# Performance work log

Measured on AMD Instinct MI355X. Metric: run time of the kernel, lower is better.

Reference implementation:

```python
import jax, jax.numpy as jnp
import numpy as np
from jax import lax

B, C, H, W = 32, 3, 128, 128   # batch, image channels, event spatial dims
PC = 16                         # conditioning distribution_params channels
HID = 64                        # hidden channels of each parallel CNN
NUP = 2                         # number of upsampling stages
DN = ('NCHW', 'OIHW', 'NCHW')

BASE_SLICE = (slice(0, None, 2), slice(0, None, 2))
UP_SLICES = [(slice(1, None, 2), slice(1, None, 2)),
             (slice(0, None, 2), slice(1, None, 2)),
             (slice(1, None, 2), slice(0, None, 2))]


def setup_inputs() -> dict:
    key = jax.random.key(0)
    k0, k1, k2, k3 = jax.random.split(key, 4)
    n_nets = C + NUP * 3 * C  # 3 base + 18 upsampling nets = 21
    cin = C + PC
    return {
        'value': jax.random.uniform(k0, (B, C, H, W), jnp.float32),
        'distribution_params': jax.random.normal(k1, (B, PC, H, W), jnp.float32),
        'W1': jax.random.normal(k2, (n_nets, HID, cin, 3, 3), jnp.float32) * 0.05,
        'b1': jnp.zeros((n_nets, HID), jnp.float32),
        'W2': jax.random.normal(k3, (n_nets, 1, HID, 1, 1), jnp.float32) * 0.05,
        'b2': jnp.zeros((n_nets, 1), jnp.float32),
    }


def _cnn(x, w1, bb1, w2, bb2):
    # Conv3x3 -> ReLU -> Conv1x1, producing Bernoulli logits [B,1,h,w]
    h = lax.conv_general_dilated(x, w1, (1, 1), 'SAME', dimension_numbers=DN)
    h = jax.nn.relu(h + bb1[None, :, None, None])
    o = lax.conv_general_dilated(h, w2, (1, 1), 'SAME', dimension_numbers=DN)
    return o + bb2[None, :, None, None]


def _log_prob_block(imgs, params, masked, sl, idxs, W1, b1, W2, b2):
    lp = jnp.float32(0.0)
    for c, idx in enumerate(idxs):
        net_in = jnp.concatenate([masked, params], axis=1)
        logits = _cnn(net_in, W1[idx], b1[idx], W2[idx], b2[idx])[:, 0, sl[0], sl[1]]
        x = imgs[:, c, sl[0], sl[1]]
        # Bernoulli log-prob with logits, summed over batch and spatial dims
        lp = lp + jnp.sum(x * jax.nn.log_sigmoid(logits)
                          + (1.0 - x) * jax.nn.log_sigmoid(-logits))
        masked = masked.at[:, c, sl[0], sl[1]].set(x)
    return lp, masked


def reference(value, distribution_params, W1, b1, W2, b2):
    r = 2 ** NUP
    base = value[:, :, ::r, ::r]
    base_dp = distribution_params[:, :, ::r, ::r]
    masked = jnp.zeros_like(base)
    lp, masked = _log_prob_block(base, base_dp, masked, BASE_SLICE,
                                 list(range(C)), W1, b1, W2, b2)
    for level in range(NUP):
        rr = 2 ** (NUP - level - 1)
        v = value[:, :, ::rr, ::rr]
        dp = distribution_params[:, :, ::rr, ::rr]
        m = jnp.zeros_like(v)
        m = m.at[:, :, BASE_SLICE[0], BASE_SLICE[1]].set(
            v[:, :, BASE_SLICE[0], BASE_SLICE[1]])
        for s in range(3):
            idxs = [C + level * 3 * C + s * C + c for c in range(C)]
            blp, m = _log_prob_block(v, dp, m, UP_SLICES[s], idxs, W1, b1, W2, b2)
            lp = lp + blp
    return lp
```

## Files before the change

### kernel.cpp

```cpp
#include <hip/hip_runtime.h>

typedef unsigned char uchar;
typedef unsigned long long ull;
typedef __attribute__((ext_vector_type(2))) unsigned long long ullx2;
typedef __attribute__((ext_vector_type(4))) float floatx4;
typedef __attribute__((ext_vector_type(4))) unsigned int uintx4;

#define NB_IMG 18496
#define WHALF 9216
#define AREG 16352

__device__ __forceinline__ uchar f2e4(float x) {
    float a = fabsf(x);
    unsigned s = (__float_as_uint(x) >> 24) & 0x80u;
    if (a >= 448.f) return (uchar)(s | 0x7E);
    if (a < 0.015625f) {
        int m = (int)rintf(a * 512.f);
        return (uchar)(s | (unsigned)m);
    }
    unsigned u = __float_as_uint(a);
    unsigned r = u + 0x7FFFFu + ((u >> 20) & 1u);
    unsigned e8 = (r >> 23) - 120u;
    return (uchar)(s | (e8 << 3) | ((r >> 20) & 7u));
}

__device__ __forceinline__ float row16sum(float v) {
    v += __int_as_float(__builtin_amdgcn_update_dpp(0, __float_as_int(v), 0x128, 0xf, 0xf, false));
    v += __int_as_float(__builtin_amdgcn_update_dpp(0, __float_as_int(v), 0x124, 0xf, 0xf, false));
    v += __int_as_float(__builtin_amdgcn_update_dpp(0, __float_as_int(v), 0x122, 0xf, 0xf, false));
    v += __int_as_float(__builtin_amdgcn_update_dpp(0, __float_as_int(v), 0x121, 0xf, 0xf, false));
    return v;
}

__device__ __forceinline__ void eval_geom(int e, int& sy0, int& sx0, int& cch, int& s_idx) {
    if (e < 3) { sy0 = 0; sx0 = 0; cch = e; s_idx = -1; }
    else {
        int u = e - 3; int s = (u % 9) / 3; cch = u % 3; s_idx = s;
        sy0 = (s == 1) ? 0 : 1;
        sx0 = (s == 2) ? 0 : 1;
    }
}

__device__ __forceinline__ bool tap_active(int e, int ci, int dy, int dx,
                                           int sy0, int sx0, int cch, int s_idx) {
    if (ci >= 3) return true;
    int py = (sy0 + dy - 1) & 1;
    int px = (sx0 + dx - 1) & 1;
    if (e < 3) return (py == 0 && px == 0) && (ci < cch);
    if (py == 0 && px == 0) return true;
    int sp = (py == 1 && px == 1) ? 0 : ((py == 0 && px == 1) ? 1 : 2);
    return (sp < s_idx) || (sp == s_idx && ci < cch);
}

__global__ __launch_bounds__(256) void prep_kernel(
    const float* __restrict__ value, const float* __restrict__ dp,
    const float* __restrict__ W1,
    uchar* __restrict__ imgbf, uchar* __restrict__ wbfA, uchar* __restrict__ wbfB,
    float* __restrict__ out)
{
    const int bid = blockIdx.x;
    if (bid < 2312) {
        const int t = bid * 256 + threadIdx.x;
        const int b = t / NB_IMG;
        const int r = t - b * NB_IMG;
        const int y = r / 136;
        const int rr = r - y * 136;
        const int p = rr / 68;
        const int xh = rr - p * 68;
        const int yi = y - 4;
        const int xi = 2 * (xh - 2) + p;
        unsigned d[8];
        #pragma unroll
        for (int i = 0; i < 8; ++i) d[i] = 0;
        if ((unsigned)yi < 128u && (unsigned)xi < 128u) {
            const int o = yi * 128 + xi;
            const float* vb = value + (size_t)b * 3 * 16384 + o;
            const float* pb = dp + (size_t)b * 16 * 16384 + o;
            #pragma unroll
            for (int i = 0; i < 3; ++i) d[i >> 2] |= (unsigned)f2e4(vb[i * 16384]) << ((i & 3) * 8);
            #pragma unroll
            for (int i = 0; i < 16; ++i) {
                const int ci = 3 + i;
                d[ci >> 2] |= (unsigned)f2e4(pb[i * 16384]) << ((ci & 3) * 8);
            }
        }
        uchar* dst = imgbf + (size_t)t * 32;
        uintx4 v0, v1;
        v0[0] = d[0]; v0[1] = d[1]; v0[2] = d[2]; v0[3] = d[3];
        v1[0] = d[4]; v1[1] = d[5]; v1[2] = d[6]; v1[3] = d[7];
        *(uintx4*)dst = v0;
        *(uintx4*)(dst + 16) = v1;
    } else {
        const int q = bid - 2312;
        const int e = q / 9, tap = q % 9;
        const int g = threadIdx.x >> 6, n = threadIdx.x & 63;
        int sy0, sx0, cch, s_idx;
        eval_geom(e, sy0, sx0, cch, s_idx);
        const int dy = tap / 3, dx = tap % 3;
        const float* wrow = W1 + ((size_t)e * 64 + n) * 171;
        ull v = 0;
        #pragma unroll
        for (int qq = 0; qq < 8; ++qq) {
            const int ci = g * 8 + qq;
            float w = 0.f;
            if (ci < 19 && tap_active(e, ci, dy, dx, sy0, sx0, cch, s_idx))
                w = wrow[ci * 9 + tap];
            v |= (ull)f2e4(w) << (qq * 8);
        }
        if (n < 32) *(ull*)&wbfA[(size_t)e * WHALF + ((tap * 4 + g) * 32 + n) * 8] = v;
        else        *(ull*)&wbfB[(size_t)e * WHALF + ((tap * 4 + g) * 32 + (n - 32)) * 8] = v;
        if (bid == 2500 && threadIdx.x == 0) out[0] = 0.f;
    }
}

struct SW { ullx2 a, b, c; };

__device__ __forceinline__ void sw_load(int tid, SW& r, const uchar* wbfB, int e) {
    const uchar* src = wbfB + (size_t)e * WHALF;
    r.a = *(const ullx2*)(src + tid * 16);
    r.b = *(const ullx2*)(src + (256 + tid) * 16);
    if (tid < 64) r.c = *(const ullx2*)(src + (512 + tid) * 16);
}
__device__ __forceinline__ void sw_write(int tid, uchar* dst, const SW& r) {
    *(ullx2*)(dst + tid * 16) = r.a;
    *(ullx2*)(dst + (256 + tid) * 16) = r.b;
    if (tid < 64) *(ullx2*)(dst + (512 + tid) * 16) = r.c;
}

template<int SY0, int SX0, int RSH, int OWSH, int TXH>
__device__ __forceinline__ void class_body(
    int e0, int e_after, SW& sw, float& lpsum,
    int b, int oy0, int ox0, int tid,
    const uchar* Alds, uchar* Wb,
    const uchar* __restrict__ wbfA, const uchar* __restrict__ wbfB,
    const float* __restrict__ value, const float* __restrict__ b1,
    const float* __restrict__ W2, const float* __restrict__ b2)
{
    constexpr int OW = 1 << OWSH;
    const int w = tid >> 6, lane = tid & 63, l15 = lane & 15, l4 = lane >> 4;
    int abase[2];
    #pragma unroll
    for (int a = 0; a < 2; ++a) {
        const int row = w * 32 + a * 16 + l15;
        const int oy = row >> OWSH, ox = row & (OW - 1);
        abase[a] = ((SY0 + 2 * oy) * 2 * TXH + ox) * 24 + l4 * 8;
    }
    const int wfb = l4 * 256 + l15 * 8;

    #pragma unroll 1
    for (int c = 0; c < 3; ++c) {
        const int e = e0 + c;
        const int en = (c < 2) ? (e + 1) : e_after;

        __syncthreads();
        sw_write(tid, Wb, sw);
        if (en >= 0) sw_load(tid, sw, wbfB, en);
        __syncthreads();

        const uchar* wA = wbfA + (size_t)e * WHALF;
        ull breg[9][2];
        #pragma unroll
        for (int tap = 0; tap < 9; ++tap) {
            breg[tap][0] = *(const ull*)(wA + tap * 1024 + wfb);
            breg[tap][1] = *(const ull*)(wA + tap * 1024 + wfb + 128);
        }
        float b1c[4], w2c[4];
        #pragma unroll
        for (int nb = 0; nb < 4; ++nb) {
            b1c[nb] = b1[e * 64 + nb * 16 + l15];
            w2c[nb] = W2[e * 64 + nb * 16 + l15];
        }
        const float bias2 = b2[e];

        floatx4 acc[2][4];
        #pragma unroll
        for (int a = 0; a < 2; ++a)
            #pragma unroll
            for (int nb = 0; nb < 4; ++nb)
                acc[a][nb] = (floatx4){0.f, 0.f, 0.f, 0.f};

        __builtin_amdgcn_s_setprio(1);
        #pragma unroll
        for (int tap = 0; tap < 9; ++tap) {
            const int dy = tap / 3, dx = tap % 3;
            const int v = SX0 + dx + 1;
            const int D = (2 * dy + (v & 1)) * TXH + (v >> 1);
            ull av[2];
            #pragma unroll
            for (int a = 0; a < 2; ++a)
                av[a] = *(const ull*)(Alds + abase[a] + D * 24);
            const ull bv2 = *(const ull*)(Wb + wfb + tap * 1024);
            const ull bv3 = *(const ull*)(Wb + wfb + tap * 1024 + 128);
            #pragma unroll
            for (int a = 0; a < 2; ++a) {
                acc[a][0] = __builtin_amdgcn_mfma_f32_16x16x32_fp8_fp8((long)av[a], (long)breg[tap][0], acc[a][0], 0, 0, 0);
                acc[a][1] = __builtin_amdgcn_mfma_f32_16x16x32_fp8_fp8((long)av[a], (long)breg[tap][1], acc[a][1], 0, 0, 0);
                acc[a][2] = __builtin_amdgcn_mfma_f32_16x16x32_fp8_fp8((long)av[a], (long)bv2, acc[a][2], 0, 0, 0);
                acc[a][3] = __builtin_amdgcn_mfma_f32_16x16x32_fp8_fp8((long)av[a], (long)bv3, acc[a][3], 0, 0, 0);
            }
        }
        __builtin_amdgcn_s_setprio(0);

        float zv[8];
        #pragma unroll
        for (int a = 0; a < 2; ++a)
            #pragma unroll
            for (int j = 0; j < 4; ++j) {
                float part = 0.f;
                #pragma unroll
                for (int nb = 0; nb < 4; ++nb)
                    part += w2c[nb] * fmaxf(acc[a][nb][j] + b1c[nb], 0.f);
                zv[a * 4 + j] = row16sum(part);
            }
        if (l15 < 8) {
            const float u0 = (l15 & 1) ? zv[1] : zv[0];
            const float u1 = (l15 & 1) ? zv[3] : zv[2];
            const float u2 = (l15 & 1) ? zv[5] : zv[4];
            const float u3 = (l15 & 1) ? zv[7] : zv[6];
            const float p0 = (l15 & 2) ? u1 : u0;
            const float p1 = (l15 & 2) ? u3 : u2;
            const float zs = ((l15 & 4) ? p1 : p0) + bias2;
            const int row = w * 32 + ((l15 >> 2) << 4) + (l4 << 2) + (l15 & 3);
            const int oyj = oy0 + (row >> OWSH);
            const int oxj = ox0 + (row & (OW - 1));
            const int yj = (SY0 + 2 * oyj) << RSH;
            const int xj = (SX0 + 2 * oxj) << RSH;
            const float xv = value[((size_t)b * 3 + c) * 16384 + yj * 128 + xj];
            const float az = fabsf(zs);
            const float t2 = __builtin_amdgcn_exp2f(-1.442695041f * az);
            const float l1p = 0.69314718056f * __builtin_amdgcn_logf(1.f + t2);
            lpsum += xv * zs + fminf(-zs, 0.f) - l1p;
        }
    }
}

template<int EB, int RSH, int OWSH, int TXH, int TY, int NCLS>
__device__ __forceinline__ void run_level(
    int b, int oy0, int ox0, int tid,
    uchar* Alds, uchar* Wb, float* wsum,
    const uchar* __restrict__ imgbf, const uchar* __restrict__ wbfA,
    const uchar* __restrict__ wbfB, const float* __restrict__ value,
    const float* __restrict__ b1, const float* __restrict__ W2,
    const float* __restrict__ b2, float* __restrict__ out)
{
    constexpr int TPIX = TY * 2 * TXH;
    const int lane = tid & 63, w = tid >> 6;

    SW sw;
    sw_load(tid, sw, wbfB, EB);

    const int yb = 2 * oy0 - 1, xb = 2 * ox0 - 2;
    const uchar* img_b = imgbf + (size_t)b * ((size_t)NB_IMG * 32);
    #pragma unroll
    for (int i = 0; i < (TPIX + 255) / 256; ++i) {
        const int px = tid + i * 256;
        if (px < TPIX) {
            const int typ = px / TXH;
            const int xh = px - typ * TXH;
            const int yl = yb + (typ >> 1);
            const int xl = xb + 2 * xh + (typ & 1);
            int yi = (yl << RSH) + 4; yi = yi < 0 ? 0 : (yi > 135 ? 135 : yi);
            int xi = (xl << RSH) + 4; xi = xi < 0 ? 0 : (xi > 135 ? 135 : xi);
            const uchar* src = img_b + (size_t)(yi * 136 + (xi & 1) * 68 + (xi >> 1)) * 32;
            ullx2 v01 = *(const ullx2*)src;
            ull v2 = *(const ull*)(src + 16);
            uchar* dst = Alds + px * 24;
            *(ull*)dst = v01[0];
            *(ull*)(dst + 8) = v01[1];
            *(ull*)(dst + 16) = v2;
        }
    }
    if (tid < 4) *(ull*)(Alds + TPIX * 24 + tid * 8) = 0ull;

    float lpsum = 0.f;
    if constexpr (NCLS == 3) {
        class_body<1, 1, RSH, OWSH, TXH>(EB + 0, EB + 3, sw, lpsum, b, oy0, ox0, tid, Alds, Wb, wbfA, wbfB, value, b1, W2, b2);
        class_body<0, 1, RSH, OWSH, TXH>(EB + 3, EB + 6, sw, lpsum, b, oy0, ox0, tid, Alds, Wb, wbfA, wbfB, value, b1, W2, b2);
        class_body<1, 0, RSH, OWSH, TXH>(EB + 6, -1, sw, lpsum, b, oy0, ox0, tid, Alds, Wb, wbfA, wbfB, value, b1, W2, b2);
    } else {
        class_body<0, 0, RSH, OWSH, TXH>(EB, -1, sw, lpsum, b, oy0, ox0, tid, Alds, Wb, wbfA, wbfB, value, b1, W2, b2);
    }

    lpsum += __shfl_down(lpsum, 32);
    lpsum += __shfl_down(lpsum, 16);
    lpsum += __shfl_down(lpsum, 8);
    lpsum += __shfl_down(lpsum, 4);
    lpsum += __shfl_down(lpsum, 2);
    lpsum += __shfl_down(lpsum, 1);
    if (lane == 0) wsum[w] = lpsum;
    __syncthreads();
    if (tid == 0) atomicAdd(out, wsum[0] + wsum[1] + wsum[2] + wsum[3]);
}

__global__ __launch_bounds__(256, 4) void pcnn_all(
    const uchar* __restrict__ imgbf, const uchar* __restrict__ wbfA,
    const uchar* __restrict__ wbfB, const float* __restrict__ value,
    const float* __restrict__ b1, const float* __restrict__ W2,
    const float* __restrict__ b2, float* __restrict__ out)
{
    __shared__ __align__(16) uchar Alds[AREG];
    __shared__ __align__(16) uchar Wb[WHALF];
    __shared__ float wsum[4];
    const int bid = blockIdx.x, tid = threadIdx.x;

    const int x = bid & 7, r = bid >> 3;
    const int g = r / 42, u = r - g * 42;
    const int b = g * 8 + x;

    if (u < 32) {
        run_level<12, 0, 5, 34, 10, 3>(b, (u >> 1) * 4, (u & 1) * 32, tid, Alds, Wb, wsum,
                                       imgbf, wbfA, wbfB, value, b1, W2, b2, out);
    } else if (u < 40) {
        run_level<3, 1, 5, 34, 10, 3>(b, (u - 32) * 4, 0, tid, Alds, Wb, wsum,
                                      imgbf, wbfA, wbfB, value, b1, W2, b2, out);
    } else {
        run_level<0, 2, 4, 17, 18, 1>(b, (u - 40) * 8, 0, tid, Alds, Wb, wsum,
                                      imgbf, wbfA, wbfB, value, b1, W2, b2, out);
    }
}

extern "C" void kernel_launch(void* const* d_in, const int* in_sizes, int n_in,
                              void* d_out, int out_size, void* d_ws, size_t ws_size,
                              hipStream_t stream) {
    const float* value = (const float*)d_in[0];
    const float* dp    = (const float*)d_in[1];
    const float* W1    = (const float*)d_in[2];
    const float* b1    = (const float*)d_in[3];
    const float* W2    = (const float*)d_in[4];
    const float* b2    = (const float*)d_in[5];
    float* out = (float*)d_out;

    uchar* imgbf = (uchar*)d_ws;
    uchar* wbfA  = imgbf + (size_t)32 * NB_IMG * 32;
    uchar* wbfB  = wbfA + (size_t)21 * WHALF;

    hipLaunchKernelGGL(prep_kernel, dim3(2501), dim3(256), 0, stream,
                       value, dp, W1, imgbf, wbfA, wbfB, out);
    hipLaunchKernelGGL(pcnn_all, dim3(1344), dim3(256), 0, stream,
                       imgbf, wbfA, wbfB, value, b1, W2, b2, out);
}
```

Measured before the change: 78.44 us.

## Split per-class network evaluations into separate blocks for more parallelism

```diff
diff --git a/kernel.cpp b/kernel.cpp
--- a/kernel.cpp
+++ b/kernel.cpp
@@ -127,116 +127,9 @@
     if (tid < 64) *(ullx2*)(dst + (512 + tid) * 16) = r.c;
 }
 
-template<int SY0, int SX0, int RSH, int OWSH, int TXH>
-__device__ __forceinline__ void class_body(
-    int e0, int e_after, SW& sw, float& lpsum,
-    int b, int oy0, int ox0, int tid,
-    const uchar* Alds, uchar* Wb,
-    const uchar* __restrict__ wbfA, const uchar* __restrict__ wbfB,
-    const float* __restrict__ value, const float* __restrict__ b1,
-    const float* __restrict__ W2, const float* __restrict__ b2)
-{
-    constexpr int OW = 1 << OWSH;
-    const int w = tid >> 6, lane = tid & 63, l15 = lane & 15, l4 = lane >> 4;
-    int abase[2];
-    #pragma unroll
-    for (int a = 0; a < 2; ++a) {
-        const int row = w * 32 + a * 16 + l15;
-        const int oy = row >> OWSH, ox = row & (OW - 1);
-        abase[a] = ((SY0 + 2 * oy) * 2 * TXH + ox) * 24 + l4 * 8;
-    }
-    const int wfb = l4 * 256 + l15 * 8;
-
-    #pragma unroll 1
-    for (int c = 0; c < 3; ++c) {
-        const int e = e0 + c;
-        const int en = (c < 2) ? (e + 1) : e_after;
-
-        __syncthreads();
-        sw_write(tid, Wb, sw);
-        if (en >= 0) sw_load(tid, sw, wbfB, en);
-        __syncthreads();
-
-        const uchar* wA = wbfA + (size_t)e * WHALF;
-        ull breg[9][2];
-        #pragma unroll
-        for (int tap = 0; tap < 9; ++tap) {
-            breg[tap][0] = *(const ull*)(wA + tap * 1024 + wfb);
-            breg[tap][1] = *(const ull*)(wA + tap * 1024 + wfb + 128);
-        }
-        float b1c[4], w2c[4];
-        #pragma unroll
-        for (int nb = 0; nb < 4; ++nb) {
-            b1c[nb] = b1[e * 64 + nb * 16 + l15];
-            w2c[nb] = W2[e * 64 + nb * 16 + l15];
-        }
-        const float bias2 = b2[e];
-
-        floatx4 acc[2][4];
-        #pragma unroll
-        for (int a = 0; a < 2; ++a)
-            #pragma unroll
-            for (int nb = 0; nb < 4; ++nb)
-                acc[a][nb] = (floatx4){0.f, 0.f, 0.f, 0.f};
-
-        __builtin_amdgcn_s_setprio(1);
-        #pragma unroll
-        for (int tap = 0; tap < 9; ++tap) {
-            const int dy = tap / 3, dx = tap % 3;
-            const int v = SX0 + dx + 1;
-            const int D = (2 * dy + (v & 1)) * TXH + (v >> 1);
-            ull av[2];
-            #pragma unroll
-            for (int a = 0; a < 2; ++a)
-                av[a] = *(const ull*)(Alds + abase[a] + D * 24);
-            const ull bv2 = *(const ull*)(Wb + wfb + tap * 1024);
-            const ull bv3 = *(const ull*)(Wb + wfb + tap * 1024 + 128);
-            #pragma unroll
-            for (int a = 0; a < 2; ++a) {
-                acc[a][0] = __builtin_amdgcn_mfma_f32_16x16x32_fp8_fp8((long)av[a], (long)breg[tap][0], acc[a][0], 0, 0, 0);
-                acc[a][1] = __builtin_amdgcn_mfma_f32_16x16x32_fp8_fp8((long)av[a], (long)breg[tap][1], acc[a][1], 0, 0, 0);
-                acc[a][2] = __builtin_amdgcn_mfma_f32_16x16x32_fp8_fp8((long)av[a], (long)bv2, acc[a][2], 0, 0, 0);
-                acc[a][3] = __builtin_amdgcn_mfma_f32_16x16x32_fp8_fp8((long)av[a], (long)bv3, acc[a][3], 0, 0, 0);
-            }
-        }
-        __builtin_amdgcn_s_setprio(0);
-
-        float zv[8];
-        #pragma unroll
-        for (int a = 0; a < 2; ++a)
-            #pragma unroll
-            for (int j = 0; j < 4; ++j) {
-                float part = 0.f;
-                #pragma unroll
-                for (int nb = 0; nb < 4; ++nb)
-                    part += w2c[nb] * fmaxf(acc[a][nb][j] + b1c[nb], 0.f);
-                zv[a * 4 + j] = row16sum(part);
-            }
-        if (l15 < 8) {
-            const float u0 = (l15 & 1) ? zv[1] : zv[0];
-            const float u1 = (l15 & 1) ? zv[3] : zv[2];
-            const float u2 = (l15 & 1) ? zv[5] : zv[4];
-            const float u3 = (l15 & 1) ? zv[7] : zv[6];
-            const float p0 = (l15 & 2) ? u1 : u0;
-            const float p1 = (l15 & 2) ? u3 : u2;
-            const float zs = ((l15 & 4) ? p1 : p0) + bias2;
-            const int row = w * 32 + ((l15 >> 2) << 4) + (l4 << 2) + (l15 & 3);
-            const int oyj = oy0 + (row >> OWSH);
-            const int oxj = ox0 + (row & (OW - 1));
-            const int yj = (SY0 + 2 * oyj) << RSH;
-            const int xj = (SX0 + 2 * oxj) << RSH;
-            const float xv = value[((size_t)b * 3 + c) * 16384 + yj * 128 + xj];
-            const float az = fabsf(zs);
-            const float t2 = __builtin_amdgcn_exp2f(-1.442695041f * az);
-            const float l1p = 0.69314718056f * __builtin_amdgcn_logf(1.f + t2);
-            lpsum += xv * zs + fminf(-zs, 0.f) - l1p;
-        }
-    }
-}
-
-template<int EB, int RSH, int OWSH, int TXH, int TY, int NCLS>
-__device__ __forceinline__ void run_level(
-    int b, int oy0, int ox0, int tid,
+template<int SY0, int SX0, int RSH, int OWSH, int TXH, int TY>
+__device__ __forceinline__ void run_eval(
+    int e, int c, int b, int oy0, int ox0, int tid,
     uchar* Alds, uchar* Wb, float* wsum,
     const uchar* __restrict__ imgbf, const uchar* __restrict__ wbfA,
     const uchar* __restrict__ wbfB, const float* __restrict__ value,
@@ -244,10 +137,13 @@
     const float* __restrict__ b2, float* __restrict__ out)
 {
     constexpr int TPIX = TY * 2 * TXH;
+    constexpr int OW = 1 << OWSH;
     const int lane = tid & 63, w = tid >> 6;
+    const int l15 = lane & 15, l4 = lane >> 4;
+    const int wfb = l4 * 256 + l15 * 8;
 
     SW sw;
-    sw_load(tid, sw, wbfB, EB);
+    sw_load(tid, sw, wbfB, e);
 
     const int yb = 2 * oy0 - 1, xb = 2 * ox0 - 2;
     const uchar* img_b = imgbf + (size_t)b * ((size_t)NB_IMG * 32);
@@ -271,14 +167,91 @@
         }
     }
     if (tid < 4) *(ull*)(Alds + TPIX * 24 + tid * 8) = 0ull;
-
+    sw_write(tid, Wb, sw);
+    __syncthreads();
+
+    const uchar* wA = wbfA + (size_t)e * WHALF;
+    ull breg[9][2];
+    #pragma unroll
+    for (int tap = 0; tap < 9; ++tap) {
+        breg[tap][0] = *(const ull*)(wA + tap * 1024 + wfb);
+        breg[tap][1] = *(const ull*)(wA + tap * 1024 + wfb + 128);
+    }
+    float b1c[4], w2c[4];
+    #pragma unroll
+    for (int nb = 0; nb < 4; ++nb) {
+        b1c[nb] = b1[e * 64 + nb * 16 + l15];
+        w2c[nb] = W2[e * 64 + nb * 16 + l15];
+    }
+    const float bias2 = b2[e];
+
+    int abase[2];
+    #pragma unroll
+    for (int a = 0; a < 2; ++a) {
+        const int row = w * 32 + a * 16 + l15;
+        const int oy = row >> OWSH, ox = row & (OW - 1);
+        abase[a] = ((SY0 + 2 * oy) * 2 * TXH + ox) * 24 + l4 * 8;
+    }
+
+    floatx4 acc[2][4];
+    #pragma unroll
+    for (int a = 0; a < 2; ++a)
+        #pragma unroll
+        for (int nb = 0; nb < 4; ++nb)
+            acc[a][nb] = (floatx4){0.f, 0.f, 0.f, 0.f};
+
+    __builtin_amdgcn_s_setprio(1);
+    #pragma unroll
+    for (int tap = 0; tap < 9; ++tap) {
+        const int dy = tap / 3, dx = tap % 3;
+        const int v = SX0 + dx + 1;
+        const int D = (2 * dy + (v & 1)) * TXH + (v >> 1);
+        ull av[2];
+        #pragma unroll
+        for (int a = 0; a < 2; ++a)
+            av[a] = *(const ull*)(Alds + abase[a] + D * 24);
+        const ull bv2 = *(const ull*)(Wb + wfb + tap * 1024);
+        const ull bv3 = *(const ull*)(Wb + wfb + tap * 1024 + 128);
+        #pragma unroll
+        for (int a = 0; a < 2; ++a) {
+            acc[a][0] = __builtin_amdgcn_mfma_f32_16x16x32_fp8_fp8((long)av[a], (long)breg[tap][0], acc[a][0], 0, 0, 0);
+            acc[a][1] = __builtin_amdgcn_mfma_f32_16x16x32_fp8_fp8((long)av[a], (long)breg[tap][1], acc[a][1], 0, 0, 0);
+            acc[a][2] = __builtin_amdgcn_mfma_f32_16x16x32_fp8_fp8((long)av[a], (long)bv2, acc[a][2], 0, 0, 0);
+            acc[a][3] = __builtin_amdgcn_mfma_f32_16x16x32_fp8_fp8((long)av[a], (long)bv3, acc[a][3], 0, 0, 0);
+        }
+    }
+    __builtin_amdgcn_s_setprio(0);
+
+    float zv[8];
+    #pragma unroll
+    for (int a = 0; a < 2; ++a)
+        #pragma unroll
+        for (int j = 0; j < 4; ++j) {
+            float part = 0.f;
+            #pragma unroll
+            for (int nb = 0; nb < 4; ++nb)
+                part += w2c[nb] * fmaxf(acc[a][nb][j] + b1c[nb], 0.f);
+            zv[a * 4 + j] = row16sum(part);
+        }
     float lpsum = 0.f;
-    if constexpr (NCLS == 3) {
-        class_body<1, 1, RSH, OWSH, TXH>(EB + 0, EB + 3, sw, lpsum, b, oy0, ox0, tid, Alds, Wb, wbfA, wbfB, value, b1, W2, b2);
-        class_body<0, 1, RSH, OWSH, TXH>(EB + 3, EB + 6, sw, lpsum, b, oy0, ox0, tid, Alds, Wb, wbfA, wbfB, value, b1, W2, b2);
-        class_body<1, 0, RSH, OWSH, TXH>(EB + 6, -1, sw, lpsum, b, oy0, ox0, tid, Alds, Wb, wbfA, wbfB, value, b1, W2, b2);
-    } else {
-        class_body<0, 0, RSH, OWSH, TXH>(EB, -1, sw, lpsum, b, oy0, ox0, tid, Alds, Wb, wbfA, wbfB, value, b1, W2, b2);
+    if (l15 < 8) {
+        const float u0 = (l15 & 1) ? zv[1] : zv[0];
+        const float u1 = (l15 & 1) ? zv[3] : zv[2];
+        const float u2 = (l15 & 1) ? zv[5] : zv[4];
+        const float u3 = (l15 & 1) ? zv[7] : zv[6];
+        const float p0 = (l15 & 2) ? u1 : u0;
+        const float p1 = (l15 & 2) ? u3 : u2;
+        const float zs = ((l15 & 4) ? p1 : p0) + bias2;
+        const int row = w * 32 + ((l15 >> 2) << 4) + (l4 << 2) + (l15 & 3);
+        const int oyj = oy0 + (row >> OWSH);
+        const int oxj = ox0 + (row & (OW - 1));
+        const int yj = (SY0 + 2 * oyj) << RSH;
+        const int xj = (SX0 + 2 * oxj) << RSH;
+        const float xv = value[((size_t)b * 3 + c) * 16384 + yj * 128 + xj];
+        const float az = fabsf(zs);
+        const float t2 = __builtin_amdgcn_exp2f(-1.442695041f * az);
+        const float l1p = 0.69314718056f * __builtin_amdgcn_logf(1.f + t2);
+        lpsum = xv * zs + fminf(-zs, 0.f) - l1p;
     }
 
     lpsum += __shfl_down(lpsum, 32);
@@ -304,18 +277,36 @@
     const int bid = blockIdx.x, tid = threadIdx.x;
 
     const int x = bid & 7, r = bid >> 3;
-    const int g = r / 42, u = r - g * 42;
+    const int g = r / 366, u = r - g * 366;
     const int b = g * 8 + x;
 
-    if (u < 32) {
-        run_level<12, 0, 5, 34, 10, 3>(b, (u >> 1) * 4, (u & 1) * 32, tid, Alds, Wb, wsum,
-                                       imgbf, wbfA, wbfB, value, b1, W2, b2, out);
-    } else if (u < 40) {
-        run_level<3, 1, 5, 34, 10, 3>(b, (u - 32) * 4, 0, tid, Alds, Wb, wsum,
-                                      imgbf, wbfA, wbfB, value, b1, W2, b2, out);
+    if (u < 288) {
+        const int sc = u >> 5, t = u & 31;
+        const int s = sc / 3, c = sc - 3 * s;
+        const int e = 12 + sc;
+        const int oy0 = (t >> 1) * 4, ox0 = (t & 1) * 32;
+        if (s == 0)
+            run_eval<1, 1, 0, 5, 34, 10>(e, c, b, oy0, ox0, tid, Alds, Wb, wsum, imgbf, wbfA, wbfB, value, b1, W2, b2, out);
+        else if (s == 1)
+            run_eval<0, 1, 0, 5, 34, 10>(e, c, b, oy0, ox0, tid, Alds, Wb, wsum, imgbf, wbfA, wbfB, value, b1, W2, b2, out);
+        else
+            run_eval<1, 0, 0, 5, 34, 10>(e, c, b, oy0, ox0, tid, Alds, Wb, wsum, imgbf, wbfA, wbfB, value, b1, W2, b2, out);
+    } else if (u < 360) {
+        const int v = u - 288;
+        const int sc = v >> 3, t = v & 7;
+        const int s = sc / 3, c = sc - 3 * s;
+        const int e = 3 + sc;
+        const int oy0 = t * 4;
+        if (s == 0)
+            run_eval<1, 1, 1, 5, 34, 10>(e, c, b, oy0, 0, tid, Alds, Wb, wsum, imgbf, wbfA, wbfB, value, b1, W2, b2, out);
+        else if (s == 1)
+            run_eval<0, 1, 1, 5, 34, 10>(e, c, b, oy0, 0, tid, Alds, Wb, wsum, imgbf, wbfA, wbfB, value, b1, W2, b2, out);
+        else
+            run_eval<1, 0, 1, 5, 34, 10>(e, c, b, oy0, 0, tid, Alds, Wb, wsum, imgbf, wbfA, wbfB, value, b1, W2, b2, out);
     } else {
-        run_level<0, 2, 4, 17, 18, 1>(b, (u - 40) * 8, 0, tid, Alds, Wb, wsum,
-                                      imgbf, wbfA, wbfB, value, b1, W2, b2, out);
+        const int v = u - 360;
+        const int c = v >> 1, t = v & 1;
+        run_eval<0, 0, 2, 4, 17, 18>(c, c, b, t * 8, 0, tid, Alds, Wb, wsum, imgbf, wbfA, wbfB, value, b1, W2, b2, out);
     }
 }
 
@@ -336,6 +327,6 @@
 
     hipLaunchKernelGGL(prep_kernel, dim3(2501), dim3(256), 0, stream,
                        value, dp, W1, imgbf, wbfA, wbfB, out);
-    hipLaunchKernelGGL(pcnn_all, dim3(1344), dim3(256), 0, stream,
+    hipLaunchKernelGGL(pcnn_all, dim3(11712), dim3(256), 0, stream,
                        imgbf, wbfA, wbfB, value, b1, W2, b2, out);
 }
```

Measured after the change: 178.8 us. 2.28x slower.
